# Kernel tuning notes

Hardware: AMD Instinct MI355X
Metric: run time of the kernel (lower is better)

Reference implementation:

```python
import jax, jax.numpy as jnp
import numpy as np

N_NODES = 50000
NUM_HYPEREDGES = 50000


def setup_inputs() -> dict:
    key = jax.random.key(0)
    k1, k2, k3, k4, k5 = jax.random.split(key, 5)
    E = 1_600_000
    F_IN, F_OUT = 128, 128
    X = jax.random.normal(k1, (N_NODES, F_IN), dtype=jnp.float32)
    nodes = jax.random.randint(k2, (E,), 0, N_NODES, dtype=jnp.int64)
    hedges = jax.random.randint(k3, (E,), 0, NUM_HYPEREDGES, dtype=jnp.int64)
    edge_index = jnp.stack([nodes, hedges], axis=0)
    W = jax.random.normal(k4, (F_IN, F_OUT), dtype=jnp.float32) * (1.0 / np.sqrt(F_IN))
    b = jax.random.normal(k5, (F_OUT,), dtype=jnp.float32) * 0.02
    return {"X": X, "edge_index": edge_index, "W": W, "b": b}


def reference(X, edge_index, W, b):
    nodes = edge_index[0]   # [E] node ids (source of incidence)
    hedges = edge_index[1]  # [E] hyperedge ids
    ones = jnp.ones(nodes.shape[0], dtype=X.dtype)

    # x = lin(X)  (Linear, bias=False inside conv)
    x = X @ W  # [N, F_out]

    # B = 1 / hyperedge degree (inf -> 0)
    deg_e = jax.ops.segment_sum(ones, hedges, num_segments=NUM_HYPEREDGES)
    B_inv = jnp.where(deg_e > 0, 1.0 / deg_e, 0.0)

    # D = 1 / node degree (unit hyperedge weights; inf -> 0)
    deg_v = jax.ops.segment_sum(ones, nodes, num_segments=N_NODES)
    D_inv = jnp.where(deg_v > 0, 1.0 / deg_v, 0.0)

    # node -> hyperedge aggregation: m_e = B_e * sum_{v in e} x_v
    m = jax.ops.segment_sum(x[nodes], hedges, num_segments=NUM_HYPEREDGES)
    m = m * B_inv[:, None]  # [M, F_out]

    # hyperedge -> node aggregation: out_v = D_v * sum_{e ni v} m_e
    out = jax.ops.segment_sum(m[hedges], nodes, num_segments=N_NODES)
    out = out * D_inv[:, None] + b  # [N, F_out]

    return jax.nn.softmax(out, axis=1)
```

## Files before the change

### kernel.cpp

```cpp
#include <hip/hip_runtime.h>
#include <hip/hip_fp16.h>

#define NN 50000
#define NM 50000
#define F  128
#define NBUK 782
#define CHSZ 8192
typedef unsigned short ushort_t;
typedef _Float16 f16;
typedef f16 f16x8 __attribute__((ext_vector_type(8)));
typedef float f32x4 __attribute__((ext_vector_type(4)));

union HF4 { float4 f4; __half2 h2[4]; };
union PK4 { uint2 u2; f16 h[4]; };

__device__ __forceinline__ int wscan64(int v, int lane) {
    int x = v;
#pragma unroll
    for (int s = 1; s < 64; s <<= 1) {
        int u = __shfl_up(x, s, 64);
        if (lane >= s) x += u;
    }
    return x;
}

__device__ __forceinline__ int bscan256(int v, int* s5, int* tot) {
    int t = threadIdx.x, lane = t & 63, wid = t >> 6;
    int incl = wscan64(v, lane);
    if (lane == 63) s5[wid] = incl;
    __syncthreads();
    if (t == 0) {
        int a = 0;
#pragma unroll
        for (int j = 0; j < 4; ++j) { int x = s5[j]; s5[j] = a; a += x; }
        s5[4] = a;
    }
    __syncthreads();
    int ex = incl - v + s5[wid];
    *tot = s5[4];
    __syncthreads();
    return ex;
}

__global__ __launch_bounds__(256) void wprep_k(const float* __restrict__ W,
                                               f16* __restrict__ Wt) {
    int i = blockIdx.x * 256 + threadIdx.x;
    int k = i >> 7, c = i & 127;
    Wt[c * 128 + k] = (f16)W[i];
}

struct GemmSmem { f16 sXh[64 * 128]; };
struct SortSmem { int hist[NBUK]; int cursor[NBUK]; int pairs[CHSZ]; int s5[5]; };
union alignas(16) FatSmem { GemmSmem g; SortSmem s; };

__global__ __launch_bounds__(256) void fat_k(const float* __restrict__ X,
                                             const f16* __restrict__ Wt,
                                             f16* __restrict__ xh,
                                             const int* __restrict__ nodes,
                                             const int* __restrict__ hedges,
                                             int* __restrict__ gchunk0, int* __restrict__ gchunk1,
                                             int* __restrict__ ghist, int* __restrict__ gstart,
                                             int E, int NCH, int nsort) {
    __shared__ FatSmem u;
    int t = threadIdx.x;

    if ((int)blockIdx.x < nsort) {
        int dir = blockIdx.x / NCH;
        int c   = blockIdx.x % NCH;
        const int* key = dir ? nodes  : hedges;
        const int* pay = dir ? hedges : nodes;
        int* gchunk    = dir ? gchunk1 : gchunk0;
        int e0 = c * CHSZ, e1 = min(E, e0 + CHSZ);

        for (int i = t; i < NBUK; i += 256) u.s.hist[i] = 0;
        __syncthreads();
        for (int e = e0 + t; e < e1; e += 256) atomicAdd(&u.s.hist[key[e] >> 6], 1);
        __syncthreads();

        int carry = 0;
        for (int base = 0; base < NBUK; base += 256) {
            int i = base + t;
            int v = (i < NBUK) ? u.s.hist[i] : 0;
            int tot;
            int ex = bscan256(v, u.s.s5, &tot);
            if (i < NBUK) u.s.cursor[i] = ex + carry;
            carry += tot;
        }
        __syncthreads();

        for (int b = t; b < NBUK; b += 256) {
            size_t idx = ((size_t)dir * NBUK + b) * NCH + c;
            ghist[idx]  = u.s.hist[b];
            gstart[idx] = u.s.cursor[b];
        }
        __syncthreads();

        for (int e = e0 + t; e < e1; e += 256) {
            int k = key[e];
            int pos = atomicAdd(&u.s.cursor[k >> 6], 1);
            u.s.pairs[pos] = ((k & 63) << 16) | pay[e];
        }
        __syncthreads();

        int n = e1 - e0;
        for (int i = t; i < n; i += 256) gchunk[(size_t)c * CHSZ + i] = u.s.pairs[i];
    } else {
        int gb = blockIdx.x - nsort;
        int row0 = gb * 64;

        const float4* X4 = (const float4*)X;
        for (int i = t; i < 64 * 32; i += 256) {
            int r = i >> 5, cq = i & 31;
            int gr = row0 + r;
            float4 xv = (gr < NN) ? X4[(size_t)gr * 32 + cq]
                                  : make_float4(0.f, 0.f, 0.f, 0.f);
            PK4 pk;
            pk.h[0] = (f16)xv.x; pk.h[1] = (f16)xv.y;
            pk.h[2] = (f16)xv.z; pk.h[3] = (f16)xv.w;
            int byte = (r * 256 + cq * 8) ^ ((r & 7) << 4);
            *(uint2*)((char*)u.g.sXh + byte) = pk.u2;
        }
        __syncthreads();

        int l = t & 63, w = t >> 6;
        int lr = l & 15, lk = l >> 4;
        f32x4 acc[8];
#pragma unroll
        for (int c = 0; c < 8; ++c) acc[c] = (f32x4){0.f, 0.f, 0.f, 0.f};

#pragma unroll
        for (int ks = 0; ks < 4; ++ks) {
            int rloc = w * 16 + lr;
            int abyte = (rloc * 256 + ks * 64 + lk * 16) ^ ((rloc & 7) << 4);
            f16x8 afrag = *(const f16x8*)((const char*)u.g.sXh + abyte);
#pragma unroll
            for (int c = 0; c < 8; ++c) {
                f16x8 bfrag = *(const f16x8*)(Wt + (c * 16 + lr) * 128 + ks * 32 + lk * 8);
                acc[c] = __builtin_amdgcn_mfma_f32_16x16x32_f16(afrag, bfrag, acc[c], 0, 0, 0);
            }
        }

#pragma unroll
        for (int c = 0; c < 8; ++c) {
            int col = c * 16 + lr;
#pragma unroll
            for (int j = 0; j < 4; ++j) {
                int row = row0 + w * 16 + lk * 4 + j;
                if (row < NN) xh[(size_t)row * 128 + col] = (f16)acc[c][j];
            }
        }
    }
}

__global__ __launch_bounds__(256) void rowsum_k(const int* __restrict__ ghist,
                                                int* __restrict__ bsum, int NCH) {
    int row = blockIdx.x * 4 + (threadIdx.x >> 6);
    int l = threadIdx.x & 63;
    if (row >= 2 * NBUK) return;
    const int* r = ghist + (size_t)row * NCH;
    int s = 0;
    for (int c = l; c < NCH; c += 64) s += r[c];
#pragma unroll
    for (int k = 32; k >= 1; k >>= 1) s += __shfl_xor(s, k, 64);
    if (l == 0) bsum[row] = s;
}

__global__ __launch_bounds__(1024) void bucketbase_k(const int* __restrict__ bsum,
                                                     int* __restrict__ bstart,
                                                     int* __restrict__ off0, int* __restrict__ off1,
                                                     int E) {
    __shared__ int s16[17];
    int dir = blockIdx.x;
    int t = threadIdx.x, lane = t & 63, wid = t >> 6;
    int v = (t < NBUK) ? bsum[dir * NBUK + t] : 0;
    int incl = wscan64(v, lane);
    if (lane == 63) s16[wid] = incl;
    __syncthreads();
    if (t < 16) {
        int x = s16[t], y = x;
#pragma unroll
        for (int s = 1; s < 16; s <<= 1) {
            int u = __shfl_up(y, s, 64);
            if (t >= s) y += u;
        }
        s16[t] = y - x;
    }
    __syncthreads();
    int ex = incl - v + s16[wid];
    if (t < NBUK) bstart[dir * NBUK + t] = ex;
    if (t == 0) (dir ? off1 : off0)[50000] = E;
}

__global__ __launch_bounds__(256) void merge_scatter_k(const int* __restrict__ gchunk0, const int* __restrict__ gchunk1,
                                                       const int* __restrict__ ghist, const int* __restrict__ gstart,
                                                       const int* __restrict__ bstart,
                                                       ushort_t* __restrict__ adj0, ushort_t* __restrict__ adj1,
                                                       int* __restrict__ off0, int* __restrict__ off1,
                                                       int NCH) {
    __shared__ int ssrc[256];
    __shared__ int sdst[257];
    __shared__ int s5[5];
    __shared__ int pairsS[CHSZ];
    __shared__ int fcnt[64], foff[64], fcur[64];

    int dir = blockIdx.x / NBUK;
    int b   = blockIdx.x % NBUK;
    int t   = threadIdx.x;
    const int* gchunk   = dir ? gchunk1 : gchunk0;
    ushort_t* adj       = dir ? adj1 : adj0;
    int* offD           = dir ? off1 : off0;

    int len = 0, src = 0;
    if (t < NCH) {
        size_t idx = ((size_t)dir * NBUK + b) * NCH + t;
        len = ghist[idx];
        src = gstart[idx];
    }
    ssrc[t] = src;
    int tot;
    int ex = bscan256(len, s5, &tot);
    sdst[t] = ex;
    if (t == 0) sdst[256] = 0x7FFFFFFF;
    if (t < 64) fcnt[t] = 0;
    __syncthreads();
    int T = tot;

    int per = (T + 255) >> 8;
    int i0 = t * per, i1 = min(T, i0 + per);
    if (i0 < i1) {
        int lo = 0, hi = 255;
        while (lo < hi) {
            int mid = (lo + hi + 1) >> 1;
            if (sdst[mid] <= i0) lo = mid; else hi = mid - 1;
        }
        int c = lo;
        for (int i = i0; i < i1; ++i) {
            while (c < 255 && sdst[c + 1] <= i) ++c;
            int p = gchunk[(size_t)c * CHSZ + ssrc[c] + (i - sdst[c])];
            pairsS[i] = p;
            atomicAdd(&fcnt[p >> 16], 1);
        }
    }
    __syncthreads();

    int bst = bstart[dir * NBUK + b];
    if (t < 64) {
        int x = fcnt[t];
        int y = wscan64(x, t);
        foff[t] = y - x;
        fcur[t] = y - x;
        int d = b * 64 + t;
        if (d < 50000) offD[d] = bst + foff[t];
    }
    __syncthreads();

    for (int i = t; i < T; i += 256) {
        int p = pairsS[i];
        int slot = atomicAdd(&fcur[p >> 16], 1);
        adj[(size_t)bst + slot] = (ushort_t)(p & 0xFFFF);
    }
}

__global__ __launch_bounds__(256) void agg_a_k(const float4* __restrict__ x4,
                                               const ushort_t* __restrict__ adj,
                                               const int* __restrict__ off,
                                               float4* __restrict__ m4) {
    int t = threadIdx.x;
    int seg = blockIdx.x * 4 + (t >> 6);
    int l = t & 63;
    int rg = l >> 4, cc = l & 15;
    int p0 = off[seg], p1 = off[seg + 1];
    float acc[8] = {};
    int i = p0;
    for (; i + 16 <= p1; i += 16) {
        int r0 = adj[i + rg], r1 = adj[i + 4 + rg], r2 = adj[i + 8 + rg], r3 = adj[i + 12 + rg];
        HF4 u0, u1, u2, u3;
        u0.f4 = x4[(size_t)r0 * 16 + cc];
        u1.f4 = x4[(size_t)r1 * 16 + cc];
        u2.f4 = x4[(size_t)r2 * 16 + cc];
        u3.f4 = x4[(size_t)r3 * 16 + cc];
#pragma unroll
        for (int k = 0; k < 4; ++k) {
            float2 f0 = __half22float2(u0.h2[k]);
            float2 f1 = __half22float2(u1.h2[k]);
            float2 f2 = __half22float2(u2.h2[k]);
            float2 f3 = __half22float2(u3.h2[k]);
            acc[2 * k]     += (f0.x + f1.x) + (f2.x + f3.x);
            acc[2 * k + 1] += (f0.y + f1.y) + (f2.y + f3.y);
        }
    }
    for (; i < p1; i += 4) {
        int r = i + rg;
        if (r < p1) {
            HF4 u;
            u.f4 = x4[(size_t)adj[r] * 16 + cc];
#pragma unroll
            for (int k = 0; k < 4; ++k) {
                float2 f = __half22float2(u.h2[k]);
                acc[2 * k] += f.x; acc[2 * k + 1] += f.y;
            }
        }
    }
#pragma unroll
    for (int k = 0; k < 8; ++k) {
        acc[k] += __shfl_xor(acc[k], 16, 64);
        acc[k] += __shfl_xor(acc[k], 32, 64);
    }
    if (l < 16) {
        float inv = (p1 > p0) ? 1.0f / (float)(p1 - p0) : 0.0f;
        HF4 w;
#pragma unroll
        for (int k = 0; k < 4; ++k)
            w.h2[k] = __floats2half2_rn(acc[2 * k] * inv, acc[2 * k + 1] * inv);
        m4[(size_t)seg * 16 + cc] = w.f4;
    }
}

__global__ __launch_bounds__(256) void agg_b_k(const float4* __restrict__ m4,
                                               const ushort_t* __restrict__ adj,
                                               const int* __restrict__ off,
                                               const float* __restrict__ bias,
                                               float4* __restrict__ out4) {
    int t = threadIdx.x;
    int seg = blockIdx.x * 4 + (t >> 6);
    int l = t & 63;
    int rg = l >> 4, cc = l & 15;
    int p0 = off[seg], p1 = off[seg + 1];
    float acc[8] = {};
    int i = p0;
    for (; i + 16 <= p1; i += 16) {
        int r0 = adj[i + rg], r1 = adj[i + 4 + rg], r2 = adj[i + 8 + rg], r3 = adj[i + 12 + rg];
        HF4 u0, u1, u2, u3;
        u0.f4 = m4[(size_t)r0 * 16 + cc];
        u1.f4 = m4[(size_t)r1 * 16 + cc];
        u2.f4 = m4[(size_t)r2 * 16 + cc];
        u3.f4 = m4[(size_t)r3 * 16 + cc];
#pragma unroll
        for (int k = 0; k < 4; ++k) {
            float2 f0 = __half22float2(u0.h2[k]);
            float2 f1 = __half22float2(u1.h2[k]);
            float2 f2 = __half22float2(u2.h2[k]);
            float2 f3 = __half22float2(u3.h2[k]);
            acc[2 * k]     += (f0.x + f1.x) + (f2.x + f3.x);
            acc[2 * k + 1] += (f0.y + f1.y) + (f2.y + f3.y);
        }
    }
    for (; i < p1; i += 4) {
        int r = i + rg;
        if (r < p1) {
            HF4 u;
            u.f4 = m4[(size_t)adj[r] * 16 + cc];
#pragma unroll
            for (int k = 0; k < 4; ++k) {
                float2 f = __half22float2(u.h2[k]);
                acc[2 * k] += f.x; acc[2 * k + 1] += f.y;
            }
        }
    }
#pragma unroll
    for (int k = 0; k < 8; ++k) {
        acc[k] += __shfl_xor(acc[k], 16, 64);
        acc[k] += __shfl_xor(acc[k], 32, 64);
    }
    float inv = (p1 > p0) ? 1.0f / (float)(p1 - p0) : 0.0f;
    const float4* b4 = (const float4*)bias;
    float4 bb0 = b4[cc * 2], bb1 = b4[cc * 2 + 1];
    float lg[8];
    lg[0] = acc[0] * inv + bb0.x; lg[1] = acc[1] * inv + bb0.y;
    lg[2] = acc[2] * inv + bb0.z; lg[3] = acc[3] * inv + bb0.w;
    lg[4] = acc[4] * inv + bb1.x; lg[5] = acc[5] * inv + bb1.y;
    lg[6] = acc[6] * inv + bb1.z; lg[7] = acc[7] * inv + bb1.w;

    float mx = lg[0];
#pragma unroll
    for (int k = 1; k < 8; ++k) mx = fmaxf(mx, lg[k]);
#pragma unroll
    for (int s = 1; s < 16; s <<= 1) mx = fmaxf(mx, __shfl_xor(mx, s, 16));
    float e[8], sm = 0.f;
#pragma unroll
    for (int k = 0; k < 8; ++k) { e[k] = __expf(lg[k] - mx); sm += e[k]; }
#pragma unroll
    for (int s = 1; s < 16; s <<= 1) sm += __shfl_xor(sm, s, 16);
    float r = 1.0f / sm;
    if (l < 16) {
        out4[(size_t)seg * 32 + cc * 2]     = make_float4(e[0] * r, e[1] * r, e[2] * r, e[3] * r);
        out4[(size_t)seg * 32 + cc * 2 + 1] = make_float4(e[4] * r, e[5] * r, e[6] * r, e[7] * r);
    }
}

extern "C" void kernel_launch(void* const* d_in, const int* in_sizes, int n_in,
                              void* d_out, int out_size, void* d_ws, size_t ws_size,
                              hipStream_t stream) {
    const float* X  = (const float*)d_in[0];
    const int*   ei = (const int*)d_in[1];
    const float* W  = (const float*)d_in[2];
    const float* b  = (const float*)d_in[3];

    int E = in_sizes[1] / 2;
    const int* nodes  = ei;
    const int* hedges = ei + E;
    int NCH = (E + CHSZ - 1) / CHSZ;
    int nsort = 2 * NCH;
    int gemmb = (NN + 63) / 64;

    char* p = (char*)d_ws;
    f16* xh = (f16*)p;                    p += (size_t)NN * F * 2;
    f16* mh = (f16*)p;                    p += (size_t)NM * F * 2;
    ushort_t* adj0 = (ushort_t*)p;        p += (size_t)E * 2;
    ushort_t* adj1 = (ushort_t*)p;        p += (size_t)E * 2;
    int* ghist  = (int*)p;                p += (size_t)2 * NBUK * NCH * 4;
    int* gstart = (int*)p;                p += (size_t)2 * NBUK * NCH * 4;
    int* bstart = (int*)p;                p += (size_t)2 * NBUK * 4;
    int* bsum   = (int*)p;                p += (size_t)2 * NBUK * 4;
    int* off0   = (int*)p;                p += (size_t)(NN + 1) * 4;
    int* off1   = (int*)p;                p += (size_t)(NN + 1) * 4;
    f16* Wt     = (f16*)p;                p += (size_t)128 * 128 * 2;
    p = (char*)(((uintptr_t)p + 15) & ~(uintptr_t)15);
    int* gchunk0 = (int*)p;
    int* gchunk1 = gchunk0 + (size_t)NCH * CHSZ;

    wprep_k<<<64, 256, 0, stream>>>(W, Wt);
    fat_k<<<nsort + gemmb, 256, 0, stream>>>(X, Wt, xh, nodes, hedges,
                                             gchunk0, gchunk1, ghist, gstart, E, NCH, nsort);
    rowsum_k<<<(2 * NBUK + 3) / 4, 256, 0, stream>>>(ghist, bsum, NCH);
    bucketbase_k<<<2, 1024, 0, stream>>>(bsum, bstart, off0, off1, E);
    merge_scatter_k<<<2 * NBUK, 256, 0, stream>>>(gchunk0, gchunk1, ghist, gstart, bstart,
                                                  adj0, adj1, off0, off1, NCH);
    agg_a_k<<<NM / 4, 256, 0, stream>>>((const float4*)xh, adj0, off0, (float4*)mh);
    agg_b_k<<<NN / 4, 256, 0, stream>>>((const float4*)mh, adj1, off1, b, (float4*)d_out);
}
```

Baseline: 182.2 us.

## Split features into 32-column slices for L2-local gathers; separate softmax pass

Stores the transformed features and hyperedge messages in four slice-major 32-column planes. Each block now gathers only one slice for eight segments, so each gathered plane is a quarter of the size and more likely to stay in L2/cache. Accumulation switches to packed fp16 adds, which is cheaper but less precise for high-degree segments. Because no block holds a full row any more, the softmax moves to a new kernel that reads fp16 logits staged in reused workspace, adding one launch and an extra round trip through memory.

```diff
diff --git a/kernel.cpp b/kernel.cpp
--- a/kernel.cpp
+++ b/kernel.cpp
@@ -142,11 +142,11 @@
 
 #pragma unroll
         for (int c = 0; c < 8; ++c) {
-            int col = c * 16 + lr;
+            size_t sbase = ((size_t)(c >> 1) * NN) * 32 + (c & 1) * 16 + lr;
 #pragma unroll
             for (int j = 0; j < 4; ++j) {
                 int row = row0 + w * 16 + lk * 4 + j;
-                if (row < NN) xh[(size_t)row * 128 + col] = (f16)acc[c][j];
+                if (row < NN) xh[sbase + (size_t)row * 32] = (f16)acc[c][j];
             }
         }
     }
@@ -261,131 +261,135 @@
     }
 }
 
-__global__ __launch_bounds__(256) void agg_a_k(const float4* __restrict__ x4,
+__global__ __launch_bounds__(256) void agg_a_k(const float4* __restrict__ xs4,
                                                const ushort_t* __restrict__ adj,
                                                const int* __restrict__ off,
-                                               float4* __restrict__ m4) {
+                                               float4* __restrict__ ms4) {
     int t = threadIdx.x;
-    int seg = blockIdx.x * 4 + (t >> 6);
+    int bid = blockIdx.x;
+    int s = (bid & 7) >> 1;
+    int seg = (bid >> 3) * 8 + (bid & 1) * 4 + (t >> 6);
     int l = t & 63;
-    int rg = l >> 4, cc = l & 15;
+    int eg = l >> 2, cl = l & 3;
     int p0 = off[seg], p1 = off[seg + 1];
-    float acc[8] = {};
+    const float4* base = xs4 + (size_t)s * NN * 4 + cl;
+    __half2 z = __floats2half2_rn(0.f, 0.f);
+    __half2 a0 = z, a1 = z, a2 = z, a3 = z;
     int i = p0;
-    for (; i + 16 <= p1; i += 16) {
-        int r0 = adj[i + rg], r1 = adj[i + 4 + rg], r2 = adj[i + 8 + rg], r3 = adj[i + 12 + rg];
-        HF4 u0, u1, u2, u3;
-        u0.f4 = x4[(size_t)r0 * 16 + cc];
-        u1.f4 = x4[(size_t)r1 * 16 + cc];
-        u2.f4 = x4[(size_t)r2 * 16 + cc];
-        u3.f4 = x4[(size_t)r3 * 16 + cc];
-#pragma unroll
-        for (int k = 0; k < 4; ++k) {
-            float2 f0 = __half22float2(u0.h2[k]);
-            float2 f1 = __half22float2(u1.h2[k]);
-            float2 f2 = __half22float2(u2.h2[k]);
-            float2 f3 = __half22float2(u3.h2[k]);
-            acc[2 * k]     += (f0.x + f1.x) + (f2.x + f3.x);
-            acc[2 * k + 1] += (f0.y + f1.y) + (f2.y + f3.y);
-        }
-    }
-    for (; i < p1; i += 4) {
-        int r = i + rg;
-        if (r < p1) {
-            HF4 u;
-            u.f4 = x4[(size_t)adj[r] * 16 + cc];
-#pragma unroll
-            for (int k = 0; k < 4; ++k) {
-                float2 f = __half22float2(u.h2[k]);
-                acc[2 * k] += f.x; acc[2 * k + 1] += f.y;
-            }
-        }
-    }
-#pragma unroll
-    for (int k = 0; k < 8; ++k) {
-        acc[k] += __shfl_xor(acc[k], 16, 64);
-        acc[k] += __shfl_xor(acc[k], 32, 64);
-    }
-    if (l < 16) {
+    for (; i + 32 <= p1; i += 32) {
+        int r0 = adj[i + eg], r1 = adj[i + 16 + eg];
+        HF4 u0, u1;
+        u0.f4 = base[(size_t)r0 * 4];
+        u1.f4 = base[(size_t)r1 * 4];
+        a0 = __hadd2(a0, u0.h2[0]); a1 = __hadd2(a1, u0.h2[1]);
+        a2 = __hadd2(a2, u0.h2[2]); a3 = __hadd2(a3, u0.h2[3]);
+        a0 = __hadd2(a0, u1.h2[0]); a1 = __hadd2(a1, u1.h2[1]);
+        a2 = __hadd2(a2, u1.h2[2]); a3 = __hadd2(a3, u1.h2[3]);
+    }
+    if (i + 16 <= p1) {
+        int r0 = adj[i + eg];
+        HF4 u0; u0.f4 = base[(size_t)r0 * 4];
+        a0 = __hadd2(a0, u0.h2[0]); a1 = __hadd2(a1, u0.h2[1]);
+        a2 = __hadd2(a2, u0.h2[2]); a3 = __hadd2(a3, u0.h2[3]);
+        i += 16;
+    }
+    if (i + eg < p1) {
+        int r0 = adj[i + eg];
+        HF4 u0; u0.f4 = base[(size_t)r0 * 4];
+        a0 = __hadd2(a0, u0.h2[0]); a1 = __hadd2(a1, u0.h2[1]);
+        a2 = __hadd2(a2, u0.h2[2]); a3 = __hadd2(a3, u0.h2[3]);
+    }
+    float2 f0 = __half22float2(a0), f1 = __half22float2(a1);
+    float2 f2 = __half22float2(a2), f3 = __half22float2(a3);
+    float v[8] = {f0.x, f0.y, f1.x, f1.y, f2.x, f2.y, f3.x, f3.y};
+#pragma unroll
+    for (int m = 4; m <= 32; m <<= 1)
+#pragma unroll
+        for (int k = 0; k < 8; ++k) v[k] += __shfl_xor(v[k], m, 64);
+    if (l < 4) {
         float inv = (p1 > p0) ? 1.0f / (float)(p1 - p0) : 0.0f;
         HF4 w;
 #pragma unroll
         for (int k = 0; k < 4; ++k)
-            w.h2[k] = __floats2half2_rn(acc[2 * k] * inv, acc[2 * k + 1] * inv);
-        m4[(size_t)seg * 16 + cc] = w.f4;
-    }
-}
-
-__global__ __launch_bounds__(256) void agg_b_k(const float4* __restrict__ m4,
+            w.h2[k] = __floats2half2_rn(v[2 * k] * inv, v[2 * k + 1] * inv);
+        ms4[((size_t)s * NM + seg) * 4 + cl] = w.f4;
+    }
+}
+
+__global__ __launch_bounds__(256) void agg_b_k(const float4* __restrict__ ms4,
                                                const ushort_t* __restrict__ adj,
                                                const int* __restrict__ off,
                                                const float* __restrict__ bias,
-                                               float4* __restrict__ out4) {
+                                               float4* __restrict__ lg4) {
     int t = threadIdx.x;
-    int seg = blockIdx.x * 4 + (t >> 6);
+    int bid = blockIdx.x;
+    int s = (bid & 7) >> 1;
+    int seg = (bid >> 3) * 8 + (bid & 1) * 4 + (t >> 6);
     int l = t & 63;
-    int rg = l >> 4, cc = l & 15;
+    int eg = l >> 2, cl = l & 3;
     int p0 = off[seg], p1 = off[seg + 1];
-    float acc[8] = {};
+    const float4* base = ms4 + (size_t)s * NM * 4 + cl;
+    __half2 z = __floats2half2_rn(0.f, 0.f);
+    __half2 a0 = z, a1 = z, a2 = z, a3 = z;
     int i = p0;
-    for (; i + 16 <= p1; i += 16) {
-        int r0 = adj[i + rg], r1 = adj[i + 4 + rg], r2 = adj[i + 8 + rg], r3 = adj[i + 12 + rg];
-        HF4 u0, u1, u2, u3;
-        u0.f4 = m4[(size_t)r0 * 16 + cc];
-        u1.f4 = m4[(size_t)r1 * 16 + cc];
-        u2.f4 = m4[(size_t)r2 * 16 + cc];
-        u3.f4 = m4[(size_t)r3 * 16 + cc];
-#pragma unroll
-        for (int k = 0; k < 4; ++k) {
-            float2 f0 = __half22float2(u0.h2[k]);
-            float2 f1 = __half22float2(u1.h2[k]);
-            float2 f2 = __half22float2(u2.h2[k]);
-            float2 f3 = __half22float2(u3.h2[k]);
-            acc[2 * k]     += (f0.x + f1.x) + (f2.x + f3.x);
-            acc[2 * k + 1] += (f0.y + f1.y) + (f2.y + f3.y);
-        }
-    }
-    for (; i < p1; i += 4) {
-        int r = i + rg;
-        if (r < p1) {
-            HF4 u;
-            u.f4 = m4[(size_t)adj[r] * 16 + cc];
-#pragma unroll
-            for (int k = 0; k < 4; ++k) {
-                float2 f = __half22float2(u.h2[k]);
-                acc[2 * k] += f.x; acc[2 * k + 1] += f.y;
-            }
-        }
-    }
-#pragma unroll
-    for (int k = 0; k < 8; ++k) {
-        acc[k] += __shfl_xor(acc[k], 16, 64);
-        acc[k] += __shfl_xor(acc[k], 32, 64);
-    }
-    float inv = (p1 > p0) ? 1.0f / (float)(p1 - p0) : 0.0f;
-    const float4* b4 = (const float4*)bias;
-    float4 bb0 = b4[cc * 2], bb1 = b4[cc * 2 + 1];
-    float lg[8];
-    lg[0] = acc[0] * inv + bb0.x; lg[1] = acc[1] * inv + bb0.y;
-    lg[2] = acc[2] * inv + bb0.z; lg[3] = acc[3] * inv + bb0.w;
-    lg[4] = acc[4] * inv + bb1.x; lg[5] = acc[5] * inv + bb1.y;
-    lg[6] = acc[6] * inv + bb1.z; lg[7] = acc[7] * inv + bb1.w;
-
-    float mx = lg[0];
-#pragma unroll
-    for (int k = 1; k < 8; ++k) mx = fmaxf(mx, lg[k]);
-#pragma unroll
-    for (int s = 1; s < 16; s <<= 1) mx = fmaxf(mx, __shfl_xor(mx, s, 16));
-    float e[8], sm = 0.f;
-#pragma unroll
-    for (int k = 0; k < 8; ++k) { e[k] = __expf(lg[k] - mx); sm += e[k]; }
-#pragma unroll
-    for (int s = 1; s < 16; s <<= 1) sm += __shfl_xor(sm, s, 16);
+    for (; i + 32 <= p1; i += 32) {
+        int r0 = adj[i + eg], r1 = adj[i + 16 + eg];
+        HF4 u0, u1;
+        u0.f4 = base[(size_t)r0 * 4];
+        u1.f4 = base[(size_t)r1 * 4];
+        a0 = __hadd2(a0, u0.h2[0]); a1 = __hadd2(a1, u0.h2[1]);
+        a2 = __hadd2(a2, u0.h2[2]); a3 = __hadd2(a3, u0.h2[3]);
+        a0 = __hadd2(a0, u1.h2[0]); a1 = __hadd2(a1, u1.h2[1]);
+        a2 = __hadd2(a2, u1.h2[2]); a3 = __hadd2(a3, u1.h2[3]);
+    }
+    if (i + 16 <= p1) {
+        int r0 = adj[i + eg];
+        HF4 u0; u0.f4 = base[(size_t)r0 * 4];
+        a0 = __hadd2(a0, u0.h2[0]); a1 = __hadd2(a1, u0.h2[1]);
+        a2 = __hadd2(a2, u0.h2[2]); a3 = __hadd2(a3, u0.h2[3]);
+        i += 16;
+    }
+    if (i + eg < p1) {
+        int r0 = adj[i + eg];
+        HF4 u0; u0.f4 = base[(size_t)r0 * 4];
+        a0 = __hadd2(a0, u0.h2[0]); a1 = __hadd2(a1, u0.h2[1]);
+        a2 = __hadd2(a2, u0.h2[2]); a3 = __hadd2(a3, u0.h2[3]);
+    }
+    float2 f0 = __half22float2(a0), f1 = __half22float2(a1);
+    float2 f2 = __half22float2(a2), f3 = __half22float2(a3);
+    float v[8] = {f0.x, f0.y, f1.x, f1.y, f2.x, f2.y, f3.x, f3.y};
+#pragma unroll
+    for (int m = 4; m <= 32; m <<= 1)
+#pragma unroll
+        for (int k = 0; k < 8; ++k) v[k] += __shfl_xor(v[k], m, 64);
+    if (l < 4) {
+        float inv = (p1 > p0) ? 1.0f / (float)(p1 - p0) : 0.0f;
+        const float4* b4 = (const float4*)bias;
+        float4 bb0 = b4[s * 8 + cl * 2];
+        float4 bb1 = b4[s * 8 + cl * 2 + 1];
+        HF4 w;
+        w.h2[0] = __floats2half2_rn(v[0] * inv + bb0.x, v[1] * inv + bb0.y);
+        w.h2[1] = __floats2half2_rn(v[2] * inv + bb0.z, v[3] * inv + bb0.w);
+        w.h2[2] = __floats2half2_rn(v[4] * inv + bb1.x, v[5] * inv + bb1.y);
+        w.h2[3] = __floats2half2_rn(v[6] * inv + bb1.z, v[7] * inv + bb1.w);
+        lg4[((size_t)s * NN + seg) * 4 + cl] = w.f4;
+    }
+}
+
+__global__ __launch_bounds__(256) void softmax_k(const __half2* __restrict__ lg2,
+                                                 float2* __restrict__ out) {
+    int seg = blockIdx.x * 4 + (threadIdx.x >> 6);
+    int l = threadIdx.x & 63;
+    float2 val = __half22float2(lg2[((size_t)(l >> 4) * NN + seg) * 16 + (l & 15)]);
+    float mx = fmaxf(val.x, val.y);
+#pragma unroll
+    for (int s2 = 32; s2 >= 1; s2 >>= 1) mx = fmaxf(mx, __shfl_xor(mx, s2, 64));
+    float e0 = __expf(val.x - mx), e1 = __expf(val.y - mx);
+    float sm = e0 + e1;
+#pragma unroll
+    for (int s2 = 32; s2 >= 1; s2 >>= 1) sm += __shfl_xor(sm, s2, 64);
     float r = 1.0f / sm;
-    if (l < 16) {
-        out4[(size_t)seg * 32 + cc * 2]     = make_float4(e[0] * r, e[1] * r, e[2] * r, e[3] * r);
-        out4[(size_t)seg * 32 + cc * 2 + 1] = make_float4(e[4] * r, e[5] * r, e[6] * r, e[7] * r);
-    }
+    out[(size_t)seg * 64 + l] = make_float2(e0 * r, e1 * r);
 }
 
 extern "C" void kernel_launch(void* const* d_in, const int* in_sizes, int n_in,
@@ -418,6 +422,7 @@
     p = (char*)(((uintptr_t)p + 15) & ~(uintptr_t)15);
     int* gchunk0 = (int*)p;
     int* gchunk1 = gchunk0 + (size_t)NCH * CHSZ;
+    f16* lgh = (f16*)gchunk0;
 
     wprep_k<<<64, 256, 0, stream>>>(W, Wt);
     fat_k<<<nsort + gemmb, 256, 0, stream>>>(X, Wt, xh, nodes, hedges,
@@ -426,6 +431,7 @@
     bucketbase_k<<<2, 1024, 0, stream>>>(bsum, bstart, off0, off1, E);
     merge_scatter_k<<<2 * NBUK, 256, 0, stream>>>(gchunk0, gchunk1, ghist, gstart, bstart,
                                                   adj0, adj1, off0, off1, NCH);
-    agg_a_k<<<NM / 4, 256, 0, stream>>>((const float4*)xh, adj0, off0, (float4*)mh);
-    agg_b_k<<<NN / 4, 256, 0, stream>>>((const float4*)mh, adj1, off1, b, (float4*)d_out);
-}
+    agg_a_k<<<NM, 256, 0, stream>>>((const float4*)xh, adj0, off0, (float4*)mh);
+    agg_b_k<<<NN, 256, 0, stream>>>((const float4*)mh, adj1, off1, b, (float4*)lgh);
+    softmax_k<<<NN / 4, 256, 0, stream>>>((const __half2*)lgh, (float2*)d_out);
+}
```

Measured after the change: 237.0 us. 1.3x slower.
